# Performance work log

Measured on AMD Instinct MI355X. Metric: run time of the kernel, lower is better.

Reference implementation:

```python
import jax, jax.numpy as jnp
import numpy as np

MASK_FILL = -99999.0  # value used by masked_fill_ in the torch source


def setup_inputs() -> dict:
    key = jax.random.key(0)
    k1, k2, k3, k4, k5, k6, k7 = jax.random.split(key, 7)
    B, S, H = 8, 2048, 1024
    query = jax.random.normal(k1, (B, S, H), dtype=jnp.float32)
    key_t = jax.random.normal(k2, (B, S, H), dtype=jnp.float32)
    value = jax.random.normal(k3, (B, S, H), dtype=jnp.float32)
    mask = jax.random.randint(k4, (B, S), 0, 2, dtype=jnp.int32)
    s = 1.0 / np.sqrt(H)
    Wq = jax.random.uniform(k5, (H, H), dtype=jnp.float32, minval=-s, maxval=s)
    Wk = jax.random.uniform(k6, (H, H), dtype=jnp.float32, minval=-s, maxval=s)
    Wv = jax.random.uniform(k7, (H, H), dtype=jnp.float32, minval=-s, maxval=s)
    return {"query": query, "key": key_t, "value": value,
            "Wq": Wq, "Wk": Wk, "Wv": Wv, "mask": mask}


def reference(query, key, value, Wq, Wk, Wv, mask):
    # Linear(h,h,bias=False): y = x @ W.T
    q = jnp.einsum('bsh,oh->bso', query, Wq)
    k = jnp.einsum('bsh,oh->bso', key, Wk)
    v = jnp.einsum('bsh,oh->bso', value, Wv)
    # score[b,i,j] = q[b,i,:] . k[b,j,:]  (NO 1/sqrt(d) scaling in source)
    score = jnp.einsum('bqh,bkh->bqk', q, k)
    # mask: [B, S_k] -> [B, 1, S_k]; positions where mask==0 get MASK_FILL
    m = mask[:, None, :]
    score = jnp.where(m == 0, jnp.float32(MASK_FILL), score)
    attn = jax.nn.softmax(score, axis=-1)
    context = jnp.einsum('bqk,bkh->bqh', attn, v)
    return context
```

## Files before the change

kernel.cpp:

```cpp
#include <hip/hip_runtime.h>
#include <hip/hip_fp16.h>
#include <math.h>

typedef _Float16 f16;
typedef _Float16 f16x4 __attribute__((ext_vector_type(4)));
typedef _Float16 f16x8 __attribute__((ext_vector_type(8)));
typedef float f32x4 __attribute__((ext_vector_type(4)));

#define GLOAD_LDS16(g, l)                                                                  \
    __builtin_amdgcn_global_load_lds((const __attribute__((address_space(1))) void*)(g),   \
                                     (__attribute__((address_space(3))) void*)(l), 16, 0, 0)

__global__ __launch_bounds__(256) void cast3_kernel(const float* __restrict__ s0,
                                                    const float* __restrict__ s1,
                                                    const float* __restrict__ s2,
                                                    f16* d0, f16* d1, f16* d2, int n4each)
{
    const int z = blockIdx.z;
    const float* src = (z == 0) ? s0 : (z == 1) ? s1 : s2;
    f16* d = (z == 0) ? d0 : (z == 1) ? d1 : d2;
    const int stride = gridDim.x * blockDim.x;
    for (int i = blockIdx.x * blockDim.x + threadIdx.x; i < n4each; i += stride) {
        float4 v = *(const float4*)(src + (long long)i * 4);
        *(f16x4*)(d + (long long)i * 4) = (f16x4){(f16)v.x, (f16)v.y, (f16)v.z, (f16)v.w};
    }
}

template <int OUTF16>
__global__ __launch_bounds__(512, 1) void gemm_nt_256(
    const f16* __restrict__ Ab, const f16* __restrict__ Bb, void* __restrict__ Cb,
    int K, int lda, int ldb, int ldc,
    long long sA, long long sB, long long sC, int gx)
{
    __shared__ __align__(16) f16 As[2][2][128 * 64];
    __shared__ __align__(16) f16 Bs[2][2][128 * 64];

    const int nwg = gridDim.x;
    const int swz = (blockIdx.x & 7) * (nwg >> 3) + (blockIdx.x >> 3);
    const int bx = swz % gx, by = swz / gx;

    const int z = blockIdx.z;
    const char* pA = (const char*)(Ab + z * sA + (long long)by * 256 * lda);
    const char* pB = (const char*)(Bb + z * sB + (long long)bx * 256 * ldb);
    const long long lda2 = (long long)lda * 2, ldb2 = (long long)ldb * 2;

    const int tid = threadIdx.x;
    const int w = tid >> 6, l = tid & 63;
    const int wr = w >> 2, wc = w & 3;

    int rs[2], cs[2];
    rs[0] = tid >> 3;
    rs[1] = (512 + tid) >> 3;
    const int cb = (tid & 7) * 16;
    cs[0] = cb ^ ((rs[0] & 7) << 4);
    cs[1] = cb ^ ((rs[1] & 7) << 4);

#define STAGE_FULL(buf, kt)                                                               \
    do {                                                                                  \
        const long long kb_ = (long long)(kt) * 128;                                      \
        _Pragma("unroll")                                                                 \
        for (int h_ = 0; h_ < 2; h_++) {                                                  \
            _Pragma("unroll")                                                             \
            for (int j_ = 0; j_ < 2; j_++) {                                              \
                GLOAD_LDS16(pA + (long long)(h_ * 128 + rs[j_]) * lda2 + kb_ + cs[j_],    \
                            &As[buf][h_][j_ * 4096 + w * 512]);                           \
                GLOAD_LDS16(pB + (long long)(h_ * 128 + rs[j_]) * ldb2 + kb_ + cs[j_],    \
                            &Bs[buf][h_][j_ * 4096 + w * 512]);                           \
            }                                                                             \
        }                                                                                 \
    } while (0)

#define FRAG(arr, buf, row256, cbyte)                                                     \
    (*(const f16x8*)((const char*)&arr[buf][0][0] + (((row256) >> 7) * 16384) +           \
                     (((row256) & 127) * 128) + ((cbyte) ^ (((row256) & 7) << 4))))

    f32x4 acc[8][4];
#pragma unroll
    for (int i = 0; i < 8; i++)
#pragma unroll
        for (int j = 0; j < 4; j++) acc[i][j] = (f32x4){0.f, 0.f, 0.f, 0.f};

    const int lr = l & 15;
    const int lkb = (l >> 4) * 16;

    const int nt = K >> 6;
    STAGE_FULL(0, 0);
    for (int t = 0; t < nt; ++t) {
        const int buf = t & 1;
        if (t + 1 < nt) {
            STAGE_FULL(buf ^ 1, t + 1);
            asm volatile("s_waitcnt vmcnt(8)" ::: "memory");
        } else {
            asm volatile("s_waitcnt vmcnt(0)" ::: "memory");
        }
        __builtin_amdgcn_s_barrier();
        __builtin_amdgcn_sched_barrier(0);

        f16x8 bf[4][2];
#pragma unroll
        for (int fc = 0; fc < 4; fc++)
#pragma unroll
            for (int ks = 0; ks < 2; ks++)
                bf[fc][ks] = FRAG(Bs, buf, wc * 64 + fc * 16 + lr, ks * 64 + lkb);

#pragma unroll
        for (int p = 0; p < 4; p++) {
            f16x8 af[2][2];
#pragma unroll
            for (int fr = 0; fr < 2; fr++)
#pragma unroll
                for (int ks = 0; ks < 2; ks++)
                    af[fr][ks] = FRAG(As, buf, wr * 128 + p * 32 + fr * 16 + lr, ks * 64 + lkb);
            __builtin_amdgcn_s_setprio(1);
#pragma unroll
            for (int fr = 0; fr < 2; fr++)
#pragma unroll
                for (int fc = 0; fc < 4; fc++)
#pragma unroll
                    for (int ks = 0; ks < 2; ks++)
                        acc[p * 2 + fr][fc] = __builtin_amdgcn_mfma_f32_16x16x32_f16(
                            af[fr][ks], bf[fc][ks], acc[p * 2 + fr][fc], 0, 0, 0);
            __builtin_amdgcn_s_setprio(0);
        }

        __builtin_amdgcn_s_barrier();
        __builtin_amdgcn_sched_barrier(0);
    }
#undef STAGE_FULL
#undef FRAG

    const int row_l = (l >> 4) * 4;
    const long long gr0 = (long long)by * 256 + wr * 128;
    const int gc0 = bx * 256 + wc * 64;
    if (OUTF16) {
        f16* C = (f16*)Cb + z * sC;
#pragma unroll
        for (int fq = 0; fq < 8; fq++)
#pragma unroll
            for (int fc = 0; fc < 4; fc++)
#pragma unroll
                for (int i = 0; i < 4; i++)
                    C[(gr0 + fq * 16 + row_l + i) * ldc + gc0 + fc * 16 + lr] = (f16)acc[fq][fc][i];
    } else {
        float* C = (float*)Cb + z * sC;
#pragma unroll
        for (int fq = 0; fq < 8; fq++)
#pragma unroll
            for (int fc = 0; fc < 4; fc++)
#pragma unroll
                for (int i = 0; i < 4; i++)
                    C[(gr0 + fq * 16 + row_l + i) * ldc + gc0 + fc * 16 + lr] = acc[fq][fc][i];
    }
}

__global__ __launch_bounds__(256) void transpose_v_kernel(const f16* __restrict__ v, f16* __restrict__ vT)
{
    __shared__ f16 tile[64][72];
    const int b = blockIdx.z;
    const int s0 = blockIdx.x * 64, o0 = blockIdx.y * 64;
    const int t = threadIdx.x;
    const int r = t >> 2, c = (t & 3) * 16;
    const f16* src = v + ((long long)b * 2048 + s0) * 1024 + o0;
    *(f16x8*)&tile[r][c]     = *(const f16x8*)(src + (long long)r * 1024 + c);
    *(f16x8*)&tile[r][c + 8] = *(const f16x8*)(src + (long long)r * 1024 + c + 8);
    __syncthreads();
    f16* dst = vT + ((long long)b * 1024 + o0) * 2048 + s0;
    f16 buf[16];
#pragma unroll
    for (int j = 0; j < 16; j++) buf[j] = tile[c + j][r];
    *(f16x8*)(dst + (long long)r * 2048 + c)     = *(f16x8*)&buf[0];
    *(f16x8*)(dst + (long long)r * 2048 + c + 8) = *(f16x8*)&buf[8];
}

__device__ __forceinline__ float wred_max(float v) {
#pragma unroll
    for (int o = 32; o > 0; o >>= 1) v = fmaxf(v, __shfl_xor(v, o));
    return v;
}
__device__ __forceinline__ float wred_sum(float v) {
#pragma unroll
    for (int o = 32; o > 0; o >>= 1) v += __shfl_xor(v, o);
    return v;
}

__global__ __launch_bounds__(256) void softmax_kernel(f16* __restrict__ Sm, const int* __restrict__ mask)
{
    const long long row = blockIdx.x;
    const int b = (int)(row >> 11);
    f16* Srow = Sm + row * 2048;
    const int* mrow = mask + b * 2048;
    const int t = threadIdx.x;
    const int w = t >> 6, l = t & 63;

    f16x8 sv = *(const f16x8*)(Srow + t * 8);
    int4 m0 = *(const int4*)(mrow + t * 8);
    int4 m1 = *(const int4*)(mrow + t * 8 + 4);
    int mk[8] = {m0.x, m0.y, m0.z, m0.w, m1.x, m1.y, m1.z, m1.w};
    float v[8];
#pragma unroll
    for (int j = 0; j < 8; j++) v[j] = (float)sv[j];

    float mx = -INFINITY;
#pragma unroll
    for (int j = 0; j < 8; j++) if (mk[j]) mx = fmaxf(mx, v[j]);
    mx = wred_max(mx);
    __shared__ float redm[4], reds[4];
    if (l == 0) redm[w] = mx;
    __syncthreads();
    mx = fmaxf(fmaxf(redm[0], redm[1]), fmaxf(redm[2], redm[3]));

    if (mx == -INFINITY) {
        const f16 u = (f16)(1.0f / 2048.0f);
        f16x8 pv;
#pragma unroll
        for (int j = 0; j < 8; j++) pv[j] = u;
        *(f16x8*)(Srow + t * 8) = pv;
        return;
    }

    float e[8];
    float s = 0.f;
#pragma unroll
    for (int j = 0; j < 8; j++) { e[j] = mk[j] ? expf(v[j] - mx) : 0.f; s += e[j]; }
    s = wred_sum(s);
    if (l == 0) reds[w] = s;
    __syncthreads();
    s = reds[0] + reds[1] + reds[2] + reds[3];
    const float inv = 1.0f / s;
    f16x8 pv;
#pragma unroll
    for (int j = 0; j < 8; j++) pv[j] = (f16)(e[j] * inv);
    *(f16x8*)(Srow + t * 8) = pv;
}

extern "C" void kernel_launch(void* const* d_in, const int* in_sizes, int n_in,
                              void* d_out, int out_size, void* d_ws, size_t ws_size,
                              hipStream_t stream)
{
    const float* query = (const float*)d_in[0];
    const float* keyi  = (const float*)d_in[1];
    const float* value = (const float*)d_in[2];
    const float* Wq    = (const float*)d_in[3];
    const float* Wk    = (const float*)d_in[4];
    const float* Wv    = (const float*)d_in[5];
    const int*   mask  = (const int*)d_in[6];
    float* out = (float*)d_out;

    const long long SH = (long long)8 * 2048 * 1024;
    f16* slot0 = (f16*)d_ws;
    f16* slot1 = slot0 + SH;
    f16* slot2 = slot0 + 2 * SH;
    f16* slot3 = slot0 + 3 * SH;
    f16* slot4 = slot0 + 4 * SH;
    f16* wh    = slot4;
    f16* Pb    = slot0;

    const int n4x = (int)(SH / 4);
    const int n4w = 1024 * 1024 / 4;
    const long long zero = 0;
    const long long M1 = 1024 * 1024;

    cast3_kernel<<<dim3(128, 1, 3), 256, 0, stream>>>(Wq, Wk, Wv, wh, wh + M1, wh + 2 * M1, n4w);
    cast3_kernel<<<dim3(2048, 1, 3), 256, 0, stream>>>(query, keyi, value, slot3, slot0, slot1, n4x);
    gemm_nt_256<1><<<dim3(256, 1, 1), 512, 0, stream>>>(
        slot3, wh, (void*)slot2, 1024, 1024, 1024, 1024, zero, zero, zero, 4);
    gemm_nt_256<1><<<dim3(256, 1, 1), 512, 0, stream>>>(
        slot0, wh + M1, (void*)slot3, 1024, 1024, 1024, 1024, zero, zero, zero, 4);
    gemm_nt_256<1><<<dim3(256, 1, 1), 512, 0, stream>>>(
        slot1, wh + 2 * M1, (void*)slot0, 1024, 1024, 1024, 1024, zero, zero, zero, 4);
    transpose_v_kernel<<<dim3(32, 16, 8), 256, 0, stream>>>(slot0, slot4);
    gemm_nt_256<1><<<dim3(64, 1, 8), 512, 0, stream>>>(
        slot2, slot3, (void*)Pb, 1024, 1024, 1024, 2048,
        (long long)2048 * 1024, (long long)2048 * 1024, (long long)2048 * 2048, 8);
    softmax_kernel<<<dim3(16384), 256, 0, stream>>>(Pb, mask);
    gemm_nt_256<0><<<dim3(32, 1, 8), 512, 0, stream>>>(
        Pb, slot4, (void*)out, 2048, 2048, 2048, 1024,
        (long long)2048 * 2048, (long long)1024 * 2048, (long long)2048 * 1024, 4);
}
```

Measured before the change: 391.4 us.

## Shrink GEMM tile to 256x128 with K-step 32 for higher occupancy

```diff
diff --git a/kernel.cpp b/kernel.cpp
--- a/kernel.cpp
+++ b/kernel.cpp
@@ -27,13 +27,13 @@
 }
 
 template <int OUTF16>
-__global__ __launch_bounds__(512, 1) void gemm_nt_256(
+__global__ __launch_bounds__(512, 4) void gemm_nt_k(
     const f16* __restrict__ Ab, const f16* __restrict__ Bb, void* __restrict__ Cb,
     int K, int lda, int ldb, int ldc,
     long long sA, long long sB, long long sC, int gx)
 {
-    __shared__ __align__(16) f16 As[2][2][128 * 64];
-    __shared__ __align__(16) f16 Bs[2][2][128 * 64];
+    __shared__ __align__(16) f16 As[2][256 * 32];
+    __shared__ __align__(16) f16 Bs[2][128 * 32];
 
     const int nwg = gridDim.x;
     const int swz = (blockIdx.x & 7) * (nwg >> 3) + (blockIdx.x >> 3);
@@ -41,101 +41,82 @@
 
     const int z = blockIdx.z;
     const char* pA = (const char*)(Ab + z * sA + (long long)by * 256 * lda);
-    const char* pB = (const char*)(Bb + z * sB + (long long)bx * 256 * ldb);
+    const char* pB = (const char*)(Bb + z * sB + (long long)bx * 128 * ldb);
     const long long lda2 = (long long)lda * 2, ldb2 = (long long)ldb * 2;
 
     const int tid = threadIdx.x;
     const int w = tid >> 6, l = tid & 63;
-    const int wr = w >> 2, wc = w & 3;
-
-    int rs[2], cs[2];
-    rs[0] = tid >> 3;
-    rs[1] = (512 + tid) >> 3;
-    const int cb = (tid & 7) * 16;
-    cs[0] = cb ^ ((rs[0] & 7) << 4);
-    cs[1] = cb ^ ((rs[1] & 7) << 4);
-
-#define STAGE_FULL(buf, kt)                                                               \
+    const int wr = w >> 1, wc = w & 1;
+
+    const int r0s = tid >> 2;
+    const int r1s = 128 + r0s;
+    const int cb = (tid & 3) * 16;
+    const int c0s = cb ^ ((r0s & 3) << 4);
+    const int c1s = cb ^ ((r1s & 3) << 4);
+
+#define STAGE(c, kt)                                                                      \
     do {                                                                                  \
-        const long long kb_ = (long long)(kt) * 128;                                      \
-        _Pragma("unroll")                                                                 \
-        for (int h_ = 0; h_ < 2; h_++) {                                                  \
-            _Pragma("unroll")                                                             \
-            for (int j_ = 0; j_ < 2; j_++) {                                              \
-                GLOAD_LDS16(pA + (long long)(h_ * 128 + rs[j_]) * lda2 + kb_ + cs[j_],    \
-                            &As[buf][h_][j_ * 4096 + w * 512]);                           \
-                GLOAD_LDS16(pB + (long long)(h_ * 128 + rs[j_]) * ldb2 + kb_ + cs[j_],    \
-                            &Bs[buf][h_][j_ * 4096 + w * 512]);                           \
-            }                                                                             \
-        }                                                                                 \
+        const long long kb_ = (long long)(kt) * 64;                                       \
+        GLOAD_LDS16(pA + (long long)r0s * lda2 + kb_ + c0s, &As[c][(long long)tid * 8]);  \
+        GLOAD_LDS16(pA + (long long)r1s * lda2 + kb_ + c1s, &As[c][(512 + (long long)tid) * 8]); \
+        GLOAD_LDS16(pB + (long long)r0s * ldb2 + kb_ + c0s, &Bs[c][(long long)tid * 8]);  \
     } while (0)
 
-#define FRAG(arr, buf, row256, cbyte)                                                     \
-    (*(const f16x8*)((const char*)&arr[buf][0][0] + (((row256) >> 7) * 16384) +           \
-                     (((row256) & 127) * 128) + ((cbyte) ^ (((row256) & 7) << 4))))
-
-    f32x4 acc[8][4];
-#pragma unroll
-    for (int i = 0; i < 8; i++)
+#define FRAG_A(c, row, kbyte)                                                             \
+    (*(const f16x8*)((const char*)&As[c][0] + ((row) * 64) + ((kbyte) ^ (((row) & 3) << 4))))
+#define FRAG_B(c, row, kbyte)                                                             \
+    (*(const f16x8*)((const char*)&Bs[c][0] + ((row) * 64) + ((kbyte) ^ (((row) & 3) << 4))))
+
+    f32x4 acc[4][4];
+#pragma unroll
+    for (int i = 0; i < 4; i++)
 #pragma unroll
         for (int j = 0; j < 4; j++) acc[i][j] = (f32x4){0.f, 0.f, 0.f, 0.f};
 
     const int lr = l & 15;
     const int lkb = (l >> 4) * 16;
 
-    const int nt = K >> 6;
-    STAGE_FULL(0, 0);
+    const int nt = K >> 5;
+    STAGE(0, 0);
     for (int t = 0; t < nt; ++t) {
         const int buf = t & 1;
         if (t + 1 < nt) {
-            STAGE_FULL(buf ^ 1, t + 1);
-            asm volatile("s_waitcnt vmcnt(8)" ::: "memory");
+            STAGE(buf ^ 1, t + 1);
+            asm volatile("s_waitcnt vmcnt(3)" ::: "memory");
         } else {
             asm volatile("s_waitcnt vmcnt(0)" ::: "memory");
         }
         __builtin_amdgcn_s_barrier();
         __builtin_amdgcn_sched_barrier(0);
 
-        f16x8 bf[4][2];
-#pragma unroll
-        for (int fc = 0; fc < 4; fc++)
-#pragma unroll
-            for (int ks = 0; ks < 2; ks++)
-                bf[fc][ks] = FRAG(Bs, buf, wc * 64 + fc * 16 + lr, ks * 64 + lkb);
-
-#pragma unroll
-        for (int p = 0; p < 4; p++) {
-            f16x8 af[2][2];
-#pragma unroll
-            for (int fr = 0; fr < 2; fr++)
-#pragma unroll
-                for (int ks = 0; ks < 2; ks++)
-                    af[fr][ks] = FRAG(As, buf, wr * 128 + p * 32 + fr * 16 + lr, ks * 64 + lkb);
-            __builtin_amdgcn_s_setprio(1);
-#pragma unroll
-            for (int fr = 0; fr < 2; fr++)
-#pragma unroll
-                for (int fc = 0; fc < 4; fc++)
-#pragma unroll
-                    for (int ks = 0; ks < 2; ks++)
-                        acc[p * 2 + fr][fc] = __builtin_amdgcn_mfma_f32_16x16x32_f16(
-                            af[fr][ks], bf[fc][ks], acc[p * 2 + fr][fc], 0, 0, 0);
-            __builtin_amdgcn_s_setprio(0);
-        }
+        f16x8 bf[4], af[4];
+#pragma unroll
+        for (int fc = 0; fc < 4; fc++) bf[fc] = FRAG_B(buf, wc * 64 + fc * 16 + lr, lkb);
+#pragma unroll
+        for (int fq = 0; fq < 4; fq++) af[fq] = FRAG_A(buf, wr * 64 + fq * 16 + lr, lkb);
+
+        __builtin_amdgcn_s_setprio(1);
+#pragma unroll
+        for (int fq = 0; fq < 4; fq++)
+#pragma unroll
+            for (int fc = 0; fc < 4; fc++)
+                acc[fq][fc] = __builtin_amdgcn_mfma_f32_16x16x32_f16(af[fq], bf[fc], acc[fq][fc], 0, 0, 0);
+        __builtin_amdgcn_s_setprio(0);
 
         __builtin_amdgcn_s_barrier();
         __builtin_amdgcn_sched_barrier(0);
     }
-#undef STAGE_FULL
-#undef FRAG
+#undef STAGE
+#undef FRAG_A
+#undef FRAG_B
 
     const int row_l = (l >> 4) * 4;
-    const long long gr0 = (long long)by * 256 + wr * 128;
-    const int gc0 = bx * 256 + wc * 64;
+    const long long gr0 = (long long)by * 256 + wr * 64;
+    const int gc0 = bx * 128 + wc * 64;
     if (OUTF16) {
         f16* C = (f16*)Cb + z * sC;
 #pragma unroll
-        for (int fq = 0; fq < 8; fq++)
+        for (int fq = 0; fq < 4; fq++)
 #pragma unroll
             for (int fc = 0; fc < 4; fc++)
 #pragma unroll
@@ -144,7 +125,7 @@
     } else {
         float* C = (float*)Cb + z * sC;
 #pragma unroll
-        for (int fq = 0; fq < 8; fq++)
+        for (int fq = 0; fq < 4; fq++)
 #pragma unroll
             for (int fc = 0; fc < 4; fc++)
 #pragma unroll
@@ -262,18 +243,18 @@
 
     cast3_kernel<<<dim3(128, 1, 3), 256, 0, stream>>>(Wq, Wk, Wv, wh, wh + M1, wh + 2 * M1, n4w);
     cast3_kernel<<<dim3(2048, 1, 3), 256, 0, stream>>>(query, keyi, value, slot3, slot0, slot1, n4x);
-    gemm_nt_256<1><<<dim3(256, 1, 1), 512, 0, stream>>>(
-        slot3, wh, (void*)slot2, 1024, 1024, 1024, 1024, zero, zero, zero, 4);
-    gemm_nt_256<1><<<dim3(256, 1, 1), 512, 0, stream>>>(
-        slot0, wh + M1, (void*)slot3, 1024, 1024, 1024, 1024, zero, zero, zero, 4);
-    gemm_nt_256<1><<<dim3(256, 1, 1), 512, 0, stream>>>(
-        slot1, wh + 2 * M1, (void*)slot0, 1024, 1024, 1024, 1024, zero, zero, zero, 4);
+    gemm_nt_k<1><<<dim3(512, 1, 1), 512, 0, stream>>>(
+        slot3, wh, (void*)slot2, 1024, 1024, 1024, 1024, zero, zero, zero, 8);
+    gemm_nt_k<1><<<dim3(512, 1, 1), 512, 0, stream>>>(
+        slot0, wh + M1, (void*)slot3, 1024, 1024, 1024, 1024, zero, zero, zero, 8);
+    gemm_nt_k<1><<<dim3(512, 1, 1), 512, 0, stream>>>(
+        slot1, wh + 2 * M1, (void*)slot0, 1024, 1024, 1024, 1024, zero, zero, zero, 8);
     transpose_v_kernel<<<dim3(32, 16, 8), 256, 0, stream>>>(slot0, slot4);
-    gemm_nt_256<1><<<dim3(64, 1, 8), 512, 0, stream>>>(
+    gemm_nt_k<1><<<dim3(128, 1, 8), 512, 0, stream>>>(
         slot2, slot3, (void*)Pb, 1024, 1024, 1024, 2048,
-        (long long)2048 * 1024, (long long)2048 * 1024, (long long)2048 * 2048, 8);
+        (long long)2048 * 1024, (long long)2048 * 1024, (long long)2048 * 2048, 16);
     softmax_kernel<<<dim3(16384), 256, 0, stream>>>(Pb, mask);
-    gemm_nt_256<0><<<dim3(32, 1, 8), 512, 0, stream>>>(
+    gemm_nt_k<0><<<dim3(64, 1, 8), 512, 0, stream>>>(
         Pb, slot4, (void*)out, 2048, 2048, 2048, 1024,
-        (long long)2048 * 2048, (long long)1024 * 2048, (long long)2048 * 1024, 4);
-}
+        (long long)2048 * 2048, (long long)1024 * 2048, (long long)2048 * 1024, 8);
+}
```

After: 380.2 us. 2.9% less time.
